# Kernel optimization log

Hardware: AMD Instinct MI355X
Metric: run time of the kernel (lower is better)

Reference implementation:

```python
import jax, jax.numpy as jnp
import numpy as np

K, S = 8, 4  # patch kernel and stride (overlapping: stride < kernel)


def _patch_idx(H, W):
    nH = (H - K) // S + 1
    nW = (W - K) // S + 1
    hh = (jnp.arange(nH) * S)[:, None] + jnp.arange(K)[None, :]  # [nH, K]
    ww = (jnp.arange(nW) * S)[:, None] + jnp.arange(K)[None, :]  # [nW, K]
    return nH, nW, hh, ww


def _split(x):
    # x: [B, C, H, W] -> [B*N, K*K, C] (same token/patch ordering as nn.Unfold)
    B, C, H, W = x.shape
    nH, nW, hh, ww = _patch_idx(H, W)
    # gather overlapping patches: [B, C, nH, nW, K, K]
    p = x[:, :, hh[:, None, :, None], ww[None, :, None, :]]
    p = jnp.transpose(p, (0, 2, 3, 4, 5, 1))  # [B, nH, nW, K, K, C]
    return p.reshape(B * nH * nW, K * K, C)


def _merge(z, B, C, H, W):
    # z: [B*N, K*K, C] -> overlap-add fold -> [B, C, H, W] (matches nn.Fold)
    nH, nW, hh, ww = _patch_idx(H, W)
    y = z.reshape(B, nH, nW, K, K, C)
    y = jnp.transpose(y, (0, 5, 1, 2, 3, 4))  # [B, C, nH, nW, K, K]
    out = jnp.zeros((B, C, H, W), z.dtype)
    out = out.at[:, :, hh[:, None, :, None], ww[None, :, None, :]].add(y)
    return out


def reference(q, k, v):
    B, C, H, W = v.shape
    qp = _split(q)  # [BN, KK, C]
    kp = _split(k)
    vp = _split(v)
    scale = C ** (-0.5)
    # per-patch attention over KK=64 tokens
    attn = jax.nn.softmax(scale * jnp.einsum('ntc,nsc->nts', qp, kp), axis=-1)
    z = jnp.einsum('nts,nsc->ntc', attn, vp)  # [BN, KK, C]
    return _merge(z, B, C, H, W)


def setup_inputs() -> dict:
    key = jax.random.key(0)
    k1, k2, k3 = jax.random.split(key, 3)
    shape = (8, 128, 128, 128)  # [B, C, H, W]
    return {
        'q': jax.random.normal(k1, shape, dtype=jnp.float32),
        'k': jax.random.normal(k2, shape, dtype=jnp.float32),
        'v': jax.random.normal(k3, shape, dtype=jnp.float32),
    }
```

## Files before the change

### kernel.cpp

```cpp
#include <hip/hip_runtime.h>

#define B_    8
#define C_    128
#define H_    128
#define W_    128
#define NH    31
#define NPB   (NH*NH)
#define NPAT  (B_*NPB)
#define HW_   (H_*W_)
#define CHW_  (C_*HW_)
#define WS_BYTES ((size_t)NPAT * 8192 * 2)

typedef float v4f __attribute__((ext_vector_type(4)));
typedef short v8s __attribute__((ext_vector_type(8)));

__device__ __forceinline__ unsigned short f2bf(float f) {
    unsigned int u = __builtin_bit_cast(unsigned int, f);
    u += 0x7FFFu + ((u >> 16) & 1u);
    return (unsigned short)(u >> 16);
}
__device__ __forceinline__ unsigned int pack2bf(float lo, float hi) {
    return (unsigned int)f2bf(lo) | ((unsigned int)f2bf(hi) << 16);
}
__device__ __forceinline__ float bfs(unsigned short u) {
    return __builtin_bit_cast(float, ((unsigned int)u) << 16);
}


__global__ __launch_bounds__(256, 5)
void patch_attn_ws(const float* __restrict__ q,
                   const float* __restrict__ k,
                   const float* __restrict__ v,
                   unsigned short* __restrict__ ws)
{
    __shared__ __align__(16) unsigned char lds[32768];
    unsigned short* sQ  = (unsigned short*)(lds);
    unsigned short* sK  = (unsigned short*)(lds + 16384);
    unsigned short* sVT = (unsigned short*)(lds);
    unsigned short* sP  = (unsigned short*)(lds + 16384);

    const int tid  = threadIdx.x;
    const int lane = tid & 63;
    const int l15  = lane & 15;
    const int quad = lane >> 4;
    const int wid  = tid >> 6;

    const int p   = (blockIdx.x & 7) * NPB + (blockIdx.x >> 3);
    const int b   = p / NPB;
    const int rem = p - b * NPB;
    const int ph  = rem / NH;
    const int pw  = rem - ph * NH;
    const int h0  = ph * 4, w0 = pw * 4;
    const int baseB = b * CHW_;

    {
        float4 qa[4], qb[4], ka[4], kb[4];
        int c0A[4], tA[4];
        #pragma unroll
        for (int g = 0; g < 4; ++g) {
            int flat2 = tid + g * 256;
            int jj = flat2 & 1;
            int i  = (flat2 >> 1) & 7;
            int cp = flat2 >> 4;
            int c0 = cp * 2;
            int off0 = baseB + c0 * HW_ + (h0 + i) * W_ + (w0 + jj * 4);
            qa[g] = *(const float4*)(q + off0);
            qb[g] = *(const float4*)(q + off0 + HW_);
            ka[g] = *(const float4*)(k + off0);
            kb[g] = *(const float4*)(k + off0 + HW_);
            c0A[g] = c0;
            tA[g]  = i * 8 + jj * 4;
        }
        #pragma unroll
        for (int g = 0; g < 4; ++g) {
            const float* fqa = (const float*)&qa[g];
            const float* fqb = (const float*)&qb[g];
            const float* fka = (const float*)&ka[g];
            const float* fkb = (const float*)&kb[g];
            int c0 = c0A[g];
            #pragma unroll
            for (int d = 0; d < 4; ++d) {
                int t = tA[g] + d;
                int chunk = (c0 >> 3) ^ (t & 15);
                int pos = t * 128 + chunk * 8 + (c0 & 7);
                *(unsigned int*)&sQ[pos] = pack2bf(fqa[d], fqb[d]);
                *(unsigned int*)&sK[pos] = pack2bf(fka[d], fkb[d]);
            }
        }
    }
    __syncthreads();

    v4f acc0, acc1, acc2, acc3;
    acc0 = acc1 = acc2 = acc3 = (v4f){0.f, 0.f, 0.f, 0.f};
    const int rowT = wid * 16 + l15;
    #pragma unroll
    for (int kk = 0; kk < 4; ++kk) {
        int gph = (kk * 4 + quad) ^ l15;
        v8s bq = *(const v8s*)(&sQ[rowT * 128 + gph * 8]);
        v8s a0 = *(const v8s*)(&sK[( 0 + l15) * 128 + gph * 8]);
        v8s a1 = *(const v8s*)(&sK[(16 + l15) * 128 + gph * 8]);
        v8s a2 = *(const v8s*)(&sK[(32 + l15) * 128 + gph * 8]);
        v8s a3 = *(const v8s*)(&sK[(48 + l15) * 128 + gph * 8]);
        acc0 = __builtin_amdgcn_mfma_f32_16x16x32_bf16(a0, bq, acc0, 0, 0, 0);
        acc1 = __builtin_amdgcn_mfma_f32_16x16x32_bf16(a1, bq, acc1, 0, 0, 0);
        acc2 = __builtin_amdgcn_mfma_f32_16x16x32_bf16(a2, bq, acc2, 0, 0, 0);
        acc3 = __builtin_amdgcn_mfma_f32_16x16x32_bf16(a3, bq, acc3, 0, 0, 0);
    }

    float4 rv[8];
    int cV[8], sV[8];
    #pragma unroll
    for (int g = 0; g < 8; ++g) {
        int flat4 = tid + g * 256;
        int jj = flat4 & 1;
        int i  = (flat4 >> 1) & 7;
        int c  = flat4 >> 4;
        rv[g] = *(const float4*)(v + baseB + c * HW_ + (h0 + i) * W_ + (w0 + jj * 4));
        cV[g] = c;
        sV[g] = i * 8 + jj * 4;
    }

    const float scale = 0.08838834764831845f;
    float e0[4], e1[4], e2[4], e3[4];
    unsigned int pPk[8];
    {
        float mx = -1e30f;
        #pragma unroll
        for (int r = 0; r < 4; ++r) {
            e0[r] = acc0[r] * scale; mx = fmaxf(mx, e0[r]);
            e1[r] = acc1[r] * scale; mx = fmaxf(mx, e1[r]);
            e2[r] = acc2[r] * scale; mx = fmaxf(mx, e2[r]);
            e3[r] = acc3[r] * scale; mx = fmaxf(mx, e3[r]);
        }
        mx = fmaxf(mx, __shfl_xor(mx, 16));
        mx = fmaxf(mx, __shfl_xor(mx, 32));
        float sum = 0.f;
        #pragma unroll
        for (int r = 0; r < 4; ++r) {
            e0[r] = __expf(e0[r] - mx); sum += e0[r];
            e1[r] = __expf(e1[r] - mx); sum += e1[r];
            e2[r] = __expf(e2[r] - mx); sum += e2[r];
            e3[r] = __expf(e3[r] - mx); sum += e3[r];
        }
        sum += __shfl_xor(sum, 16);
        sum += __shfl_xor(sum, 32);
        float inv = 1.0f / sum;
        pPk[0] = pack2bf(e0[0] * inv, e0[1] * inv);
        pPk[1] = pack2bf(e0[2] * inv, e0[3] * inv);
        pPk[2] = pack2bf(e1[0] * inv, e1[1] * inv);
        pPk[3] = pack2bf(e1[2] * inv, e1[3] * inv);
        pPk[4] = pack2bf(e2[0] * inv, e2[1] * inv);
        pPk[5] = pack2bf(e2[2] * inv, e2[3] * inv);
        pPk[6] = pack2bf(e3[0] * inv, e3[1] * inv);
        pPk[7] = pack2bf(e3[2] * inv, e3[3] * inv);
    }
    __syncthreads();

    #pragma unroll
    for (int g = 0; g < 8; ++g) {
        const float* fv = (const float*)&rv[g];
        int c = cV[g], s0 = sV[g];
        int kV = (c & 3) | (((c >> 3) & 1) << 2);
        unsigned int w0p = pack2bf(fv[0], fv[1]);
        unsigned int w1p = pack2bf(fv[2], fv[3]);
        int idx = c * 64 + ((((s0 >> 3) ^ kV) << 3) | (s0 & 7));
        uint2 val; val.x = w0p; val.y = w1p;
        *(uint2*)(&sVT[idx]) = val;
    }

    {
        const int t = rowT;
        const int qh = quad >> 1, ql = quad & 1;
        #pragma unroll
        for (int m = 0; m < 4; ++m) {
            int chunk = (m * 2 + qh) ^ (t & 7);
            uint2 val;
            val.x = pPk[m * 2];
            val.y = pPk[m * 2 + 1];
            *(uint2*)(&sP[t * 64 + chunk * 8 + ql * 4]) = val;
        }
    }
    __syncthreads();

    v4f z00, z01, z02, z03, z10, z11, z12, z13;
    z00 = z01 = z02 = z03 = (v4f){0.f, 0.f, 0.f, 0.f};
    z10 = z11 = z12 = z13 = (v4f){0.f, 0.f, 0.f, 0.f};
    const int wb = wid * 32;
    const int rA = wb + (l15 & 3) + ((l15 >> 2) << 3);
    #pragma unroll
    for (int kk = 0; kk < 2; ++kk) {
        int gph = (kk * 4 + quad) ^ (l15 & 7);
        v8s b0 = *(const v8s*)(&sP[( 0 + l15) * 64 + gph * 8]);
        v8s b1 = *(const v8s*)(&sP[(16 + l15) * 64 + gph * 8]);
        v8s b2 = *(const v8s*)(&sP[(32 + l15) * 64 + gph * 8]);
        v8s b3 = *(const v8s*)(&sP[(48 + l15) * 64 + gph * 8]);
        v8s aA = *(const v8s*)(&sVT[rA * 64 + gph * 8]);
        v8s aB = *(const v8s*)(&sVT[(rA + 4) * 64 + gph * 8]);
        z00 = __builtin_amdgcn_mfma_f32_16x16x32_bf16(aA, b0, z00, 0, 0, 0);
        z01 = __builtin_amdgcn_mfma_f32_16x16x32_bf16(aA, b1, z01, 0, 0, 0);
        z02 = __builtin_amdgcn_mfma_f32_16x16x32_bf16(aA, b2, z02, 0, 0, 0);
        z03 = __builtin_amdgcn_mfma_f32_16x16x32_bf16(aA, b3, z03, 0, 0, 0);
        z10 = __builtin_amdgcn_mfma_f32_16x16x32_bf16(aB, b0, z10, 0, 0, 0);
        z11 = __builtin_amdgcn_mfma_f32_16x16x32_bf16(aB, b1, z11, 0, 0, 0);
        z12 = __builtin_amdgcn_mfma_f32_16x16x32_bf16(aB, b2, z12, 0, 0, 0);
        z13 = __builtin_amdgcn_mfma_f32_16x16x32_bf16(aB, b3, z13, 0, 0, 0);
    }

    {
        unsigned short* wp = ws + (size_t)p * 8192 + wb + quad * 8;
        uint4 val;
        int t;
        t = 0 + l15;
        val.x = pack2bf(z00[0], z00[1]); val.y = pack2bf(z00[2], z00[3]);
        val.z = pack2bf(z10[0], z10[1]); val.w = pack2bf(z10[2], z10[3]);
        *(uint4*)(wp + t * 128) = val;
        t = 16 + l15;
        val.x = pack2bf(z01[0], z01[1]); val.y = pack2bf(z01[2], z01[3]);
        val.z = pack2bf(z11[0], z11[1]); val.w = pack2bf(z11[2], z11[3]);
        *(uint4*)(wp + t * 128) = val;
        t = 32 + l15;
        val.x = pack2bf(z02[0], z02[1]); val.y = pack2bf(z02[2], z02[3]);
        val.z = pack2bf(z12[0], z12[1]); val.w = pack2bf(z12[2], z12[3]);
        *(uint4*)(wp + t * 128) = val;
        t = 48 + l15;
        val.x = pack2bf(z03[0], z03[1]); val.y = pack2bf(z03[2], z03[3]);
        val.z = pack2bf(z13[0], z13[1]); val.w = pack2bf(z13[2], z13[3]);
        *(uint4*)(wp + t * 128) = val;
    }
}


#define MSLOT 264
#define MARR  (33 * MSLOT)

__global__ __launch_bounds__(256, 4)
void merge_kernel(const unsigned short* __restrict__ ws,
                  float* __restrict__ out)
{
    __shared__ __align__(16) unsigned short sM[2 * MARR];
    unsigned short* sA = sM;
    unsigned short* sB = sM + MARR;

    const int tid  = threadIdx.x;
    const int b    = blockIdx.x & 7;
    const int rest = blockIdx.x >> 3;
    const int hq   = rest >> 4;
    const int cg   = rest & 15;

    if (tid < 132) {
        int target = tid / 33;
        int j      = tid - target * 33;
        unsigned short* base = ((target < 2) ? sA : sB)
                             + ((target & 1) ? 32 * MSLOT : 0);
        uint4 zz; zz.x = 0u; zz.y = 0u; zz.z = 0u; zz.w = 0u;
        *(uint4*)(base + j * 8) = zz;
    }

    const int aValid = (hq <= 30);
    const int bValid = (hq >= 1);
    const int hqB = bValid ? (hq - 1) : 0;
    const size_t rowA = (size_t)(b * NPB + hq  * NH) * 8192;
    const size_t rowB = (size_t)(b * NPB + hqB * NH) * 8192;

    #pragma unroll
    for (int it = 0; it < 8; ++it) {
        int flat = tid + it * 256;
        if (flat < 1984) {
            int half = (flat >= 992);
            int fl   = flat - (half ? 992 : 0);
            int pw   = fl >> 5;
            int t    = fl & 31;
            const unsigned short* src = ws
                + (half ? rowB : rowA)
                + (size_t)pw * 8192
                + (size_t)(half ? (t + 32) : t) * 128
                + cg * 8;
            int valid = half ? bValid : aValid;
            uint4 val;
            if (valid) {
                val = *(const uint4*)src;
            } else {
                val.x = 0u; val.y = 0u; val.z = 0u; val.w = 0u;
            }
            unsigned short* dst = (half ? sB : sA)
                + (pw + 1) * MSLOT + t * 8;
            *(uint4*)dst = val;
        }
    }
    __syncthreads();

    const int l    = tid & 31;
    const int csub = tid >> 5;
    const int c    = cg * 8 + csub;

    const int own  = (l + 1) * MSLOT + csub;
    const int left = l       * MSLOT + csub;

    float* op = out + b * CHW_ + c * HW_ + (hq * 4) * W_ + l * 4;
    #pragma unroll
    for (int hr = 0; hr < 4; ++hr) {
        float rr[4];
        #pragma unroll
        for (int j = 0; j < 4; ++j) {
            int tl = hr * 8 + j;
            float s = bfs(sA[own  + tl * 8])
                    + bfs(sA[left + (tl + 4) * 8])
                    + bfs(sB[own  + tl * 8])
                    + bfs(sB[left + (tl + 4) * 8]);
            rr[j] = s;
        }
        float4 r; r.x = rr[0]; r.y = rr[1]; r.z = rr[2]; r.w = rr[3];
        *(float4*)(op + hr * W_) = r;
    }
}


__global__ __launch_bounds__(512, 6)
void patch_attn_atomic(const float* __restrict__ q,
                       const float* __restrict__ k,
                       const float* __restrict__ v,
                       float* __restrict__ out)
{
    __shared__ __align__(16) unsigned char lds[43264];
    unsigned short* sQ   = (unsigned short*)(lds);
    unsigned short* sK   = (unsigned short*)(lds + 16384);
    unsigned short* sVT  = (unsigned short*)(lds);
    unsigned short* sP   = (unsigned short*)(lds + 32768);
    float*          sRedM= (float*)(lds + 40960);
    float*          sRedL= (float*)(lds + 41984);
    float*          sInv = (float*)(lds + 43008);

    const int tid  = threadIdx.x;
    const int lane = tid & 63;
    const int wid  = tid >> 6;
    const int l15  = lane & 15;
    const int quad = lane >> 4;

    const int p   = (blockIdx.x & 7) * NPB + (blockIdx.x >> 3);
    const int b   = p / NPB;
    const int rem = p - b * NPB;
    const int ph  = rem / NH;
    const int pw  = rem - ph * NH;
    const int h0  = ph * 4, w0 = pw * 4;
    const int baseB = b * CHW_;

    float4 rq[4], rk[4], rv[4];
    int cA[4], tA[4];
    #pragma unroll
    for (int g = 0; g < 4; ++g) {
        int flat4 = tid + g * 512;
        int jj = flat4 & 1;
        int i  = (flat4 >> 1) & 7;
        int c  = flat4 >> 4;
        int off = baseB + c * HW_ + (h0 + i) * W_ + (w0 + jj * 4);
        rq[g] = *(const float4*)(q + off);
        rk[g] = *(const float4*)(k + off);
        rv[g] = *(const float4*)(v + off);
        cA[g] = c;
        tA[g] = i * 8 + jj * 4;
    }
    #pragma unroll
    for (int g = 0; g < 4; ++g) {
        const float* fq = (const float*)&rq[g];
        const float* fk = (const float*)&rk[g];
        int c = cA[g];
        #pragma unroll
        for (int d = 0; d < 4; ++d) {
            int t = tA[g] + d;
            int idx = t * 128 + ((((c >> 3) ^ (t & 15)) << 3) | (c & 7));
            sQ[idx] = f2bf(fq[d]);
            sK[idx] = f2bf(fk[d]);
        }
    }
    __syncthreads();

    const float scale = 0.08838834764831845f;
    const int nt  = wid & 3;
    const int mt0 = wid >> 2;

    v4f accT[2];
    #pragma unroll
    for (int ti = 0; ti < 2; ++ti) {
        int mt = mt0 + ti * 2;
        v4f acc = {0.f, 0.f, 0.f, 0.f};
        int rowA = mt * 16 + l15;
        int rowB = nt * 16 + l15;
        #pragma unroll
        for (int kk = 0; kk < 4; ++kk) {
            int gph = (kk * 4 + quad) ^ l15;
            v8s a  = *(const v8s*)(&sQ[rowA * 128 + gph * 8]);
            v8s bb = *(const v8s*)(&sK[rowB * 128 + gph * 8]);
            acc = __builtin_amdgcn_mfma_f32_16x16x32_bf16(a, bb, acc, 0, 0, 0);
        }
        #pragma unroll
        for (int r = 0; r < 4; ++r) acc[r] *= scale;
        accT[ti] = acc;
    }

    float4 mloc[2], eV[2];
    #pragma unroll
    for (int ti = 0; ti < 2; ++ti) {
        float4 m;
        #pragma unroll
        for (int r = 0; r < 4; ++r) m[r] = accT[ti][r];
        #pragma unroll
        for (int mask = 1; mask <= 8; mask <<= 1)
            #pragma unroll
            for (int r = 0; r < 4; ++r) m[r] = fmaxf(m[r], __shfl_xor(m[r], mask));
        float4 e, l;
        #pragma unroll
        for (int r = 0; r < 4; ++r) { e[r] = __expf(accT[ti][r] - m[r]); l[r] = e[r]; }
        #pragma unroll
        for (int mask = 1; mask <= 8; mask <<= 1)
            #pragma unroll
            for (int r = 0; r < 4; ++r) l[r] += __shfl_xor(l[r], mask);
        mloc[ti] = m; eV[ti] = e;
        if (l15 == 0) {
            int tb = (mt0 + ti * 2) * 16 + quad * 4;
            #pragma unroll
            for (int r = 0; r < 4; ++r) {
                sRedM[nt * 64 + tb + r] = m[r];
                sRedL[nt * 64 + tb + r] = l[r];
            }
        }
    }
    __syncthreads();

    #pragma unroll
    for (int g = 0; g < 4; ++g) {
        const float* fv = (const float*)&rv[g];
        unsigned short tmp[4];
        #pragma unroll
        for (int d = 0; d < 4; ++d) tmp[d] = f2bf(fv[d]);
        int c = cA[g], s0 = tA[g];
        int idx = c * 64 + ((((s0 >> 3) ^ (c & 7)) << 3) | (s0 & 7));
        *(uint2*)(&sVT[idx]) = *(const uint2*)tmp;
    }

    #pragma unroll
    for (int ti = 0; ti < 2; ++ti) {
        int tb = (mt0 + ti * 2) * 16 + quad * 4;
        float4 Mv[4], Lv[4];
        #pragma unroll
        for (int n2 = 0; n2 < 4; ++n2) {
            Mv[n2] = *(const float4*)(&sRedM[n2 * 64 + tb]);
            Lv[n2] = *(const float4*)(&sRedL[n2 * 64 + tb]);
        }
        float4 M = Mv[0], L;
        #pragma unroll
        for (int n2 = 1; n2 < 4; ++n2)
            #pragma unroll
            for (int r = 0; r < 4; ++r) M[r] = fmaxf(M[r], Mv[n2][r]);
        #pragma unroll
        for (int r = 0; r < 4; ++r) L[r] = 0.f;
        #pragma unroll
        for (int n2 = 0; n2 < 4; ++n2)
            #pragma unroll
            for (int r = 0; r < 4; ++r) L[r] += Lv[n2][r] * __expf(Mv[n2][r] - M[r]);
        #pragma unroll
        for (int r = 0; r < 4; ++r) {
            float pv = eV[ti][r] * __expf(mloc[ti][r] - M[r]);
            int t = tb + r;
            int s = nt * 16 + l15;
            sP[t * 64 + ((((s >> 3) ^ (t & 7)) << 3) | (s & 7))] = f2bf(pv);
        }
        if (nt == 0 && l15 == 0) {
            #pragma unroll
            for (int r = 0; r < 4; ++r) sInv[tb + r] = 1.0f / L[r];
        }
    }
    __syncthreads();

    v4f z[4];
    #pragma unroll
    for (int n2 = 0; n2 < 4; ++n2) z[n2] = (v4f){0.f, 0.f, 0.f, 0.f};
    const int crow = wid * 16 + l15;
    #pragma unroll
    for (int kk = 0; kk < 2; ++kk) {
        int gph = (kk * 4 + quad) ^ (l15 & 7);
        v8s a = *(const v8s*)(&sVT[crow * 64 + gph * 8]);
        #pragma unroll
        for (int n2 = 0; n2 < 4; ++n2) {
            int trow = n2 * 16 + l15;
            v8s bb = *(const v8s*)(&sP[trow * 64 + gph * 8]);
            z[n2] = __builtin_amdgcn_mfma_f32_16x16x32_bf16(a, bb, z[n2], 0, 0, 0);
        }
    }

    #pragma unroll
    for (int n2 = 0; n2 < 4; ++n2) {
        int t = n2 * 16 + l15;
        float inv = sInv[t];
        int base2 = baseB + (h0 + (t >> 3)) * W_ + (w0 + (t & 7));
        #pragma unroll
        for (int r = 0; r < 4; ++r) {
            int c = wid * 16 + quad * 4 + r;
            unsafeAtomicAdd(out + base2 + c * HW_, z[n2][r] * inv);
        }
    }
}

extern "C" void kernel_launch(void* const* d_in, const int* in_sizes, int n_in,
                              void* d_out, int out_size, void* d_ws, size_t ws_size,
                              hipStream_t stream) {
    const float* q = (const float*)d_in[0];
    const float* k = (const float*)d_in[1];
    const float* v = (const float*)d_in[2];
    float* out = (float*)d_out;

    if (ws_size >= WS_BYTES) {
        unsigned short* ws = (unsigned short*)d_ws;
        patch_attn_ws<<<NPAT, 256, 0, stream>>>(q, k, v, ws);
        merge_kernel<<<8 * 32 * 16, 256, 0, stream>>>(ws, out);
    } else {
        hipMemsetAsync(out, 0, (size_t)out_size * sizeof(float), stream);
        patch_attn_atomic<<<NPAT, 512, 0, stream>>>(q, k, v, out);
    }
}
```

Baseline: 363.4 us.

## Restructure merge kernel to tile by width segment with swizzled LDS layout

The merge kernel now gives each block a 4-patch width segment across all 128 channels, instead of a full patch row for 8 channels. It loads whole contiguous half-patch rows (4 KB each) with 16-byte reads into an XOR-swizzled LDS layout, so global reads are fully contiguous instead of 16-byte strided pieces. Each thread reads 16-byte vectors of 8 channels and unpacks pairs of bf16 values. Output stores change from float4 along W to scalar stores across 8 channel planes, coalesced across 16 lanes. LDS use rises to 80 KB per block, which lowers occupancy, and the overlap halo patches are loaded redundantly by neighbouring segments.

```diff
diff --git a/kernel.cpp b/kernel.cpp
--- a/kernel.cpp
+++ b/kernel.cpp
@@ -22,8 +22,11 @@
 __device__ __forceinline__ unsigned int pack2bf(float lo, float hi) {
     return (unsigned int)f2bf(lo) | ((unsigned int)f2bf(hi) << 16);
 }
-__device__ __forceinline__ float bfs(unsigned short u) {
-    return __builtin_bit_cast(float, ((unsigned int)u) << 16);
+__device__ __forceinline__ float bflo(unsigned int d) {
+    return __builtin_bit_cast(float, d << 16);
+}
+__device__ __forceinline__ float bfhi(unsigned int d) {
+    return __builtin_bit_cast(float, d & 0xFFFF0000u);
 }
 
 
@@ -230,87 +233,85 @@
 }
 
 
-#define MSLOT 264
-#define MARR  (33 * MSLOT)
-
-__global__ __launch_bounds__(256, 4)
+#define SLOT_U16 4096
+
+__global__ __launch_bounds__(256, 2)
 void merge_kernel(const unsigned short* __restrict__ ws,
                   float* __restrict__ out)
 {
-    __shared__ __align__(16) unsigned short sM[2 * MARR];
-    unsigned short* sA = sM;
-    unsigned short* sB = sM + MARR;
+    __shared__ __align__(16) unsigned short sM[10 * SLOT_U16];
 
     const int tid  = threadIdx.x;
     const int b    = blockIdx.x & 7;
     const int rest = blockIdx.x >> 3;
-    const int hq   = rest >> 4;
-    const int cg   = rest & 15;
-
-    if (tid < 132) {
-        int target = tid / 33;
-        int j      = tid - target * 33;
-        unsigned short* base = ((target < 2) ? sA : sB)
-                             + ((target & 1) ? 32 * MSLOT : 0);
-        uint4 zz; zz.x = 0u; zz.y = 0u; zz.z = 0u; zz.w = 0u;
-        *(uint4*)(base + j * 8) = zz;
-    }
+    const int hq   = rest >> 3;
+    const int wseg = rest & 7;
+    const int l0   = wseg * 4;
 
     const int aValid = (hq <= 30);
     const int bValid = (hq >= 1);
-    const int hqB = bValid ? (hq - 1) : 0;
-    const size_t rowA = (size_t)(b * NPB + hq  * NH) * 8192;
-    const size_t rowB = (size_t)(b * NPB + hqB * NH) * 8192;
-
-    #pragma unroll
-    for (int it = 0; it < 8; ++it) {
+    const size_t rowA = (size_t)(b * NPB + hq * NH) * 8192;
+    const size_t rowB = (size_t)(b * NPB + (bValid ? hq - 1 : 0) * NH) * 8192;
+
+    #pragma unroll
+    for (int it = 0; it < 20; ++it) {
         int flat = tid + it * 256;
-        if (flat < 1984) {
-            int half = (flat >= 992);
-            int fl   = flat - (half ? 992 : 0);
-            int pw   = fl >> 5;
-            int t    = fl & 31;
-            const unsigned short* src = ws
-                + (half ? rowB : rowA)
-                + (size_t)pw * 8192
-                + (size_t)(half ? (t + 32) : t) * 128
-                + cg * 8;
-            int valid = half ? bValid : aValid;
-            uint4 val;
-            if (valid) {
-                val = *(const uint4*)src;
-            } else {
-                val.x = 0u; val.y = 0u; val.z = 0u; val.w = 0u;
-            }
-            unsigned short* dst = (half ? sB : sA)
-                + (pw + 1) * MSLOT + t * 8;
-            *(uint4*)dst = val;
-        }
-    }
-    __syncthreads();
-
-    const int l    = tid & 31;
-    const int csub = tid >> 5;
-    const int c    = cg * 8 + csub;
-
-    const int own  = (l + 1) * MSLOT + csub;
-    const int left = l       * MSLOT + csub;
-
-    float* op = out + b * CHW_ + c * HW_ + (hq * 4) * W_ + l * 4;
+        int half = (flat >= 2560);
+        int r    = flat - (half ? 2560 : 0);
+        int slot = r >> 9;
+        int ci   = r & 511;
+        int t    = ci >> 4;
+        int kc   = ci & 15;
+        int pw   = l0 - 1 + slot;
+        int valid = (pw >= 0) & (pw <= 30) & (half ? bValid : aValid);
+        uint4 val; val.x = 0u; val.y = 0u; val.z = 0u; val.w = 0u;
+        if (valid) {
+            const unsigned short* src = ws + (half ? rowB : rowA)
+                + (size_t)pw * 8192 + (half ? 4096 : 0) + ci * 8;
+            val = *(const uint4*)src;
+        }
+        int kcs = kc ^ (((slot & 3) << 2) | (t & 3));
+        unsigned short* dst = sM + (half * 5 + slot) * SLOT_U16 + t * 128 + kcs * 8;
+        *(uint4*)dst = val;
+    }
+    __syncthreads();
+
+    const int w16  = tid & 15;
+    const int kc   = tid >> 4;
+    const int j    = w16 & 3;
+    const int sOwn = (w16 >> 2) + 1;
+    const int sLft = (w16 >> 2);
+    const int c0   = kc * 8;
+
+    const int gO = ((sOwn & 3) << 2) | j;
+    const int gL = ((sLft & 3) << 2) | j;
+
+    float* opBase = out + b * CHW_ + c0 * HW_ + (hq * 4) * W_ + wseg * 16 + w16;
+
     #pragma unroll
     for (int hr = 0; hr < 4; ++hr) {
-        float rr[4];
-        #pragma unroll
-        for (int j = 0; j < 4; ++j) {
-            int tl = hr * 8 + j;
-            float s = bfs(sA[own  + tl * 8])
-                    + bfs(sA[left + (tl + 4) * 8])
-                    + bfs(sB[own  + tl * 8])
-                    + bfs(sB[left + (tl + 4) * 8]);
-            rr[j] = s;
-        }
-        float4 r; r.x = rr[0]; r.y = rr[1]; r.z = rr[2]; r.w = rr[3];
-        *(float4*)(op + hr * W_) = r;
+        int t1 = hr * 8 + j;
+        int t2 = t1 + 4;
+        const unsigned short* aO = sM +  sOwn      * SLOT_U16 + t1 * 128 + (kc ^ gO) * 8;
+        const unsigned short* aL = sM +  sLft      * SLOT_U16 + t2 * 128 + (kc ^ gL) * 8;
+        const unsigned short* bO = sM + (5 + sOwn) * SLOT_U16 + t1 * 128 + (kc ^ gO) * 8;
+        const unsigned short* bL = sM + (5 + sLft) * SLOT_U16 + t2 * 128 + (kc ^ gL) * 8;
+        uint4 vaO = *(const uint4*)aO;
+        uint4 vaL = *(const uint4*)aL;
+        uint4 vbO = *(const uint4*)bO;
+        uint4 vbL = *(const uint4*)bL;
+        const unsigned int* uaO = (const unsigned int*)&vaO;
+        const unsigned int* uaL = (const unsigned int*)&vaL;
+        const unsigned int* ubO = (const unsigned int*)&vbO;
+        const unsigned int* ubL = (const unsigned int*)&vbL;
+        float* op = opBase + hr * W_;
+        #pragma unroll
+        for (int i = 0; i < 4; ++i) {
+            float rlo = bflo(uaO[i]) + bflo(uaL[i]) + bflo(ubO[i]) + bflo(ubL[i]);
+            float rhi = bfhi(uaO[i]) + bfhi(uaL[i]) + bfhi(ubO[i]) + bfhi(ubL[i]);
+            op[(2 * i)     * HW_] = rlo;
+            op[(2 * i + 1) * HW_] = rhi;
+        }
     }
 }
 
@@ -511,7 +512,7 @@
     if (ws_size >= WS_BYTES) {
         unsigned short* ws = (unsigned short*)d_ws;
         patch_attn_ws<<<NPAT, 256, 0, stream>>>(q, k, v, ws);
-        merge_kernel<<<8 * 32 * 16, 256, 0, stream>>>(ws, out);
+        merge_kernel<<<8 * 32 * 8, 256, 0, stream>>>(ws, out);
     } else {
         hipMemsetAsync(out, 0, (size_t)out_size * sizeof(float), stream);
         patch_attn_atomic<<<NPAT, 512, 0, stream>>>(q, k, v, out);
```

Result: no change. 356.5 us (-1.9%).
